# Kernel tuning notes

Measured on AMD Instinct MI355X. Metric: run time of the kernel, lower is better.

Reference implementation:

```python
import jax, jax.numpy as jnp
import numpy as np

N_HEAD = 16
NEG = 1e10


def setup_inputs() -> dict:
    key = jax.random.key(0)
    k1, k2, k3 = jax.random.split(key, 3)
    nx = 1024
    B, S = 2, 2048
    x = jax.random.normal(k1, (B, S, nx), dtype=jnp.float32)
    w_attn = jax.random.normal(k2, (nx, 3 * nx), dtype=jnp.float32) * (1.0 / np.sqrt(nx))
    b_attn = jnp.zeros((3 * nx,), dtype=jnp.float32)
    w_proj = jax.random.normal(k3, (nx, nx), dtype=jnp.float32) * (1.0 / np.sqrt(nx))
    b_proj = jnp.zeros((nx,), dtype=jnp.float32)
    return {"x": x, "w_attn": w_attn, "b_attn": b_attn, "w_proj": w_proj, "b_proj": b_proj}


def reference(x, w_attn, b_attn, w_proj, b_proj):
    B, S, nx = x.shape
    d = nx // N_HEAD
    qkv = x @ w_attn + b_attn                      # [B,S,3*nx]
    q, k, v = jnp.split(qkv, 3, axis=-1)
    # split heads: [B,S,nx] -> [B,H,S,d]
    q = q.reshape(B, S, N_HEAD, d).transpose(0, 2, 1, 3)
    k = k.reshape(B, S, N_HEAD, d).transpose(0, 2, 1, 3)
    v = v.reshape(B, S, N_HEAD, d).transpose(0, 2, 1, 3)
    # present: stack of (key stored as [B,H,S,d], value) like torch code
    present = jnp.stack((k, v))                    # [2,B,H,S,d]
    # scores with scale and additive causal mask (GPT-2 style: w*b - 1e10*(1-b))
    w = jnp.einsum('bhqd,bhkd->bhqk', q, k) / jnp.sqrt(jnp.float32(d))
    mask = jnp.tril(jnp.ones((S, S), dtype=w.dtype))[None, None]
    w = w * mask - NEG * (1.0 - mask)
    w = jax.nn.softmax(w, axis=-1)
    a = jnp.einsum('bhqk,bhkd->bhqd', w, v)        # [B,H,S,d]
    a = a.transpose(0, 2, 1, 3).reshape(B, S, nx)  # merge heads
    a = a @ w_proj + b_proj
    return (a, present)
```

## Files before the change

kernel.cpp:

```cpp
#include <hip/hip_runtime.h>
#include <stdint.h>
#include <stddef.h>

#define DEVI __device__ __forceinline__

typedef __bf16 bf16x8 __attribute__((ext_vector_type(8)));
typedef float  f32x4  __attribute__((ext_vector_type(4)));
typedef float  f32x16 __attribute__((ext_vector_type(16)));
typedef unsigned short u16;
typedef uint32_t u32;
typedef u16 u16x8 __attribute__((ext_vector_type(8)));
typedef u16 u16x4 __attribute__((ext_vector_type(4)));
typedef u32 u32x2 __attribute__((ext_vector_type(2)));
typedef u32 u32x4 __attribute__((ext_vector_type(4)));

typedef __attribute__((address_space(1))) void as1_void;
typedef __attribute__((address_space(3))) void as3_void;

static constexpr float SC = 0.18033688011112042f;

DEVI u16 f2bf(float f) {
  uint32_t u = __builtin_bit_cast(uint32_t, f);
  u += 0x7fffu + ((u >> 16) & 1u);
  return (u16)(u >> 16);
}

DEVI void gload_lds16(const void* g, void* l) {
  __builtin_amdgcn_global_load_lds((as1_void*)(void*)g, (as3_void*)l, 16, 0, 0);
}

#if __has_builtin(__builtin_amdgcn_exp2f)
DEVI float fast_exp2(float x) { return __builtin_amdgcn_exp2f(x); }
#else
DEVI float fast_exp2(float x) { return exp2f(x); }
#endif

DEVI u32 cvtpk(float lo, float hi) {
  u32 r;
  asm("v_cvt_pk_bf16_f32 %0, %1, %2" : "=v"(r) : "v"(lo), "v"(hi));
  return r;
}
DEVI void plswap(u32& a, u32& b) {
  asm("v_permlane32_swap_b32 %0, %1" : "+v"(a), "+v"(b));
}

__global__ __launch_bounds__(256) void k_cvt(const float* __restrict__ in,
                                             u16* __restrict__ out, int n) {
  int i = (blockIdx.x * 256 + threadIdx.x) * 4;
  if (i >= n) return;
  const float4 v = *(const float4*)(in + i);
  u16x4 o = { f2bf(v.x), f2bf(v.y), f2bf(v.z), f2bf(v.w) };
  *(u16x4*)(out + i) = o;
}

__global__ __launch_bounds__(256) void k_tcvt(const float* __restrict__ in,
                                              u16* __restrict__ out, int R, int C) {
  __shared__ float tile[32][33];
  const int c0 = blockIdx.x * 32, r0 = blockIdx.y * 32;
  const int tx = threadIdx.x, ty = threadIdx.y;
#pragma unroll
  for (int i = ty; i < 32; i += 8)
    tile[i][tx] = in[(size_t)(r0 + i) * C + (c0 + tx)];
  __syncthreads();
#pragma unroll
  for (int i = ty; i < 32; i += 8)
    out[(size_t)(c0 + i) * R + (r0 + tx)] = f2bf(tile[tx][i]);
}

__global__ __launch_bounds__(256) void k_vt(const u16* __restrict__ in,
                                            u16* __restrict__ out) {
  __shared__ u16 tile[64][72];
  const int tid = threadIdx.x;
  const int s0 = blockIdx.x * 64;
  const int bh = blockIdx.y;
  const size_t ib = (size_t)bh * 131072;
#pragma unroll
  for (int it = 0; it < 2; ++it) {
    const int r = (tid >> 3) + it * 32;
    const int c8 = (tid & 7) * 8;
    u16x8 v = *(const u16x8*)(in + ib + (size_t)(s0 + r) * 64 + c8);
    *(u16x8*)&tile[r][c8] = v;
  }
  __syncthreads();
#pragma unroll
  for (int it = 0; it < 2; ++it) {
    const int d = (tid >> 3) + it * 32;
    const int s8 = (tid & 7) * 8;
    u16x8 v;
#pragma unroll
    for (int jj = 0; jj < 8; ++jj) v[jj] = tile[s8 + jj][d];
    *(u16x8*)(out + ib + (size_t)d * 2048 + s0 + s8) = v;
  }
}

template <int EPI>
__global__ __launch_bounds__(256) void k_gemm(
    const u16* __restrict__ A, const u16* __restrict__ Bt,
    const float* __restrict__ bias,
    u16* __restrict__ wq, u16* __restrict__ wk, u16* __restrict__ wv,
    float* __restrict__ pk, float* __restrict__ pv, float* __restrict__ of) {
  constexpr int K = 1024;
  constexpr int NT = K / 32;
  __shared__ __align__(16) u16 Ash[3][128 * 32];
  __shared__ __align__(16) u16 Bsh[3][128 * 32];
  const int tid = threadIdx.x;
  const int lane = tid & 63, wid = tid >> 6;
  const int wm = wid >> 1, wn = wid & 1;
  const int lr = lane & 15, lg = lane >> 4;

  const int nwgx = gridDim.x;
  const int nwg = nwgx * gridDim.y;
  int lbid = blockIdx.y * nwgx + blockIdx.x;
  lbid = (lbid & 7) * (nwg >> 3) + (lbid >> 3);
  const int m0 = (lbid / nwgx) * 128, n0 = (lbid % nwgx) * 128;

  const int c = wid * 64 + lane;
  const u16* Ag1 = A + (size_t)(m0 + (c >> 2)) * K + (c & 3) * 8;
  const u16* Ag2 = A + (size_t)(m0 + 64 + (c >> 2)) * K + (c & 3) * 8;
  const u16* Bg1 = Bt + (size_t)(n0 + (c >> 2)) * K + (c & 3) * 8;
  const u16* Bg2 = Bt + (size_t)(n0 + 64 + (c >> 2)) * K + (c & 3) * 8;

  f32x4 acc[4][4];
#pragma unroll
  for (int i = 0; i < 4; ++i)
#pragma unroll
    for (int j = 0; j < 4; ++j) acc[i][j] = (f32x4)0.0f;

#define STAGE(sel, kk)                                        \
  {                                                           \
    gload_lds16(Ag1 + (kk), &Ash[sel][wid * 512]);            \
    gload_lds16(Ag2 + (kk), &Ash[sel][2048 + wid * 512]);     \
    gload_lds16(Bg1 + (kk), &Bsh[sel][wid * 512]);            \
    gload_lds16(Bg2 + (kk), &Bsh[sel][2048 + wid * 512]);     \
  }

  STAGE(0, 0)
  STAGE(1, 32)
  asm volatile("s_waitcnt vmcnt(4)" ::: "memory");
  __builtin_amdgcn_sched_barrier(0);
  __builtin_amdgcn_s_barrier();
  __builtin_amdgcn_sched_barrier(0);

  int cur = 0;
  for (int j = 0; j < NT; ++j) {
    const bool pf = (j + 2 < NT);
    int nb = cur + 2; if (nb >= 3) nb -= 3;
    if (pf) STAGE(nb, (j + 2) * 32)
    bf16x8 af[4], bfr[4];
#pragma unroll
    for (int f = 0; f < 4; ++f) {
      af[f]  = *(const bf16x8*)&Ash[cur][(wm * 64 + f * 16 + lr) * 32 + lg * 8];
      bfr[f] = *(const bf16x8*)&Bsh[cur][(wn * 64 + f * 16 + lr) * 32 + lg * 8];
    }
    __builtin_amdgcn_s_setprio(1);
#pragma unroll
    for (int i = 0; i < 4; ++i)
#pragma unroll
      for (int jj = 0; jj < 4; ++jj)
        acc[i][jj] = __builtin_amdgcn_mfma_f32_16x16x32_bf16(af[i], bfr[jj], acc[i][jj], 0, 0, 0);
    __builtin_amdgcn_s_setprio(0);
    if (pf) asm volatile("s_waitcnt vmcnt(4)" ::: "memory");
    else    asm volatile("s_waitcnt vmcnt(0)" ::: "memory");
    __builtin_amdgcn_sched_barrier(0);
    __builtin_amdgcn_s_barrier();
    __builtin_amdgcn_sched_barrier(0);
    cur = (cur + 1 == 3) ? 0 : cur + 1;
  }
#undef STAGE

  if constexpr (EPI == 0) {
#pragma unroll
    for (int j = 0; j < 4; ++j) {
      const int n = n0 + wn * 64 + j * 16 + lr;
      const float bv = bias[n];
      const int sec = n >> 10;
      const int nn = n & 1023;
      const int h = nn >> 6, dd = nn & 63;
#pragma unroll
      for (int i = 0; i < 4; ++i) {
        const int mb = m0 + wm * 64 + i * 16 + lg * 4;
        const int bb = mb >> 11, ss = mb & 2047;
        const size_t ib = (size_t)(bb * 16 + h) * 131072 + (size_t)ss * 64 + dd;
        if (sec == 0) {
#pragma unroll
          for (int r = 0; r < 4; ++r)
            wq[ib + (size_t)r * 64] = f2bf(acc[i][j][r] + bv);
        } else if (sec == 1) {
#pragma unroll
          for (int r = 0; r < 4; ++r) {
            const float v = acc[i][j][r] + bv;
            wk[ib + (size_t)r * 64] = f2bf(v);
            pk[ib + (size_t)r * 64] = v;
          }
        } else {
#pragma unroll
          for (int r = 0; r < 4; ++r) {
            const float v = acc[i][j][r] + bv;
            wv[ib + (size_t)r * 64] = f2bf(v);
            pv[ib + (size_t)r * 64] = v;
          }
        }
      }
    }
  } else {
#pragma unroll
    for (int j = 0; j < 4; ++j) {
      const int n = n0 + wn * 64 + j * 16 + lr;
      const float bv = bias[n];
#pragma unroll
      for (int i = 0; i < 4; ++i) {
        const int mb = m0 + wm * 64 + i * 16 + lg * 4;
#pragma unroll
        for (int r = 0; r < 4; ++r)
          of[(size_t)(mb + r) * 1024 + n] = acc[i][j][r] + bv;
      }
    }
  }
}

__global__ __launch_bounds__(128) void k_attn(const u16* __restrict__ Q,
                                              const u16* __restrict__ Kp,
                                              const u16* __restrict__ VT,
                                              u16* __restrict__ AO) {
  __shared__ __align__(16) u16 Ksh[2][4096];
  __shared__ __align__(16) u16 Vsh[2][4096];

  const int tid = threadIdx.x;
  const int lane = tid & 63, w = tid >> 6;
  const int l31 = lane & 31, hi = lane >> 5;
  const int bid = blockIdx.x;
  const int bh = bid & 31;
  const int j4 = bid >> 8;
  const int g  = (bid >> 5) & 7;
  const int qt = (j4 == 0) ? (31 - g) : (j4 == 1) ? g : (j4 == 2) ? (23 - g) : (8 + g);
  const int b = bh >> 4, h = bh & 15;
  const size_t hb = (size_t)bh * (2048 * 64);

  const int T = qt + 1;
  const int qb = qt * 64 + w * 32;

  const int srow = w * 32 + (lane >> 3);
  const int sslot = (lane & 7) ^ (lane >> 3);
  const u16* Kg = Kp + hb + (size_t)srow * 64 + sslot * 8;
  const u16* Vg = VT + hb + (size_t)srow * 2048 + sslot * 8;

#define STAGEA(sel, jt)                                                       \
  {                                                                           \
    gload_lds16(Kg + (size_t)(jt) * 4096,          &Ksh[sel][w * 2048]);      \
    gload_lds16(Kg + (size_t)(jt) * 4096 + 512,    &Ksh[sel][w * 2048 + 512]);\
    gload_lds16(Kg + (size_t)(jt) * 4096 + 1024,   &Ksh[sel][w * 2048 + 1024]);\
    gload_lds16(Kg + (size_t)(jt) * 4096 + 1536,   &Ksh[sel][w * 2048 + 1536]);\
    gload_lds16(Vg + (size_t)(jt) * 64,            &Vsh[sel][w * 2048]);      \
    gload_lds16(Vg + (size_t)(jt) * 64 + 16384,    &Vsh[sel][w * 2048 + 512]);\
    gload_lds16(Vg + (size_t)(jt) * 64 + 32768,    &Vsh[sel][w * 2048 + 1024]);\
    gload_lds16(Vg + (size_t)(jt) * 64 + 49152,    &Vsh[sel][w * 2048 + 1536]);\
  }

  const u16* Qp = Q + hb + (size_t)(qb + l31) * 64 + hi * 8;
  const bf16x8 qf0 = *(const bf16x8*)(Qp);
  const bf16x8 qf1 = *(const bf16x8*)(Qp + 16);
  const bf16x8 qf2 = *(const bf16x8*)(Qp + 32);
  const bf16x8 qf3 = *(const bf16x8*)(Qp + 48);

  f32x16 o0 = (f32x16)0.0f, o1 = (f32x16)0.0f;
  float mrun = -1e30f, lrun = 0.0f;

  const int xr = l31 & 7;

  STAGEA(0, 0)
  __syncthreads();

  int sel = 0;
  for (int jt = 0; jt < T; ++jt) {
    if (jt + 1 < T) STAGEA(sel ^ 1, jt + 1)
    const u16* Kb = Ksh[sel];
    const u16* Vb = Vsh[sel];
    bf16x8 kf[2][4];
#pragma unroll
    for (int s = 0; s < 2; ++s)
#pragma unroll
      for (int c = 0; c < 4; ++c)
        kf[s][c] = *(const bf16x8*)&Kb[(s * 32 + l31) * 64 + (((2 * c + hi) ^ xr) * 8)];

    f32x16 s0 = (f32x16)0.0f, s1 = (f32x16)0.0f;
    __builtin_amdgcn_s_setprio(1);
    s0 = __builtin_amdgcn_mfma_f32_32x32x16_bf16(kf[0][0], qf0, s0, 0, 0, 0);
    s1 = __builtin_amdgcn_mfma_f32_32x32x16_bf16(kf[1][0], qf0, s1, 0, 0, 0);
    s0 = __builtin_amdgcn_mfma_f32_32x32x16_bf16(kf[0][1], qf1, s0, 0, 0, 0);
    s1 = __builtin_amdgcn_mfma_f32_32x32x16_bf16(kf[1][1], qf1, s1, 0, 0, 0);
    s0 = __builtin_amdgcn_mfma_f32_32x32x16_bf16(kf[0][2], qf2, s0, 0, 0, 0);
    s1 = __builtin_amdgcn_mfma_f32_32x32x16_bf16(kf[1][2], qf2, s1, 0, 0, 0);
    s0 = __builtin_amdgcn_mfma_f32_32x32x16_bf16(kf[0][3], qf3, s0, 0, 0, 0);
    s1 = __builtin_amdgcn_mfma_f32_32x32x16_bf16(kf[1][3], qf3, s1, 0, 0, 0);
    __builtin_amdgcn_s_setprio(0);

    if (jt == T - 1) {
      const int qrel = w * 32 + l31;
      const int h4 = hi * 4;
#pragma unroll
      for (int r = 0; r < 16; ++r) {
        const int kp = (r & 3) + ((r >> 2) << 3) + h4;
        s0[r] = (kp <= qrel) ? s0[r] : -1e30f;
        s1[r] = (kp + 32 <= qrel) ? s1[r] : -1e30f;
      }
    }

    float t8[8];
#pragma unroll
    for (int r = 0; r < 8; ++r)
      t8[r] = fmaxf(fmaxf(s0[r], s0[r + 8]), fmaxf(s1[r], s1[r + 8]));
    float tm = fmaxf(fmaxf(fmaxf(t8[0], t8[1]), fmaxf(t8[2], t8[3])),
                     fmaxf(fmaxf(t8[4], t8[5]), fmaxf(t8[6], t8[7])));
    tm = fmaxf(tm, __shfl_xor(tm, 32));
    if (!__all(tm <= mrun)) {
      const float mnew = fmaxf(mrun, tm);
      const float al = fast_exp2((mrun - mnew) * SC);
      mrun = mnew;
      lrun *= al;
#pragma unroll
      for (int r = 0; r < 16; ++r) { o0[r] *= al; o1[r] *= al; }
    }
    const float nb2 = -mrun * SC;
#pragma unroll
    for (int r = 0; r < 16; ++r) {
      s0[r] = fast_exp2(fmaf(s0[r], SC, nb2));
      s1[r] = fast_exp2(fmaf(s1[r], SC, nb2));
    }
    float u8[8];
#pragma unroll
    for (int r = 0; r < 8; ++r)
      u8[r] = (s0[r] + s0[r + 8]) + (s1[r] + s1[r + 8]);
    lrun += ((u8[0] + u8[1]) + (u8[2] + u8[3])) + ((u8[4] + u8[5]) + (u8[6] + u8[7]));

    bf16x8 pb0, pb1, pb2, pb3;
#define PACK_CHUNK(sv, bb, dst)                                   \
    {                                                             \
      u32 a0 = cvtpk(sv[bb + 0], sv[bb + 1]);                     \
      u32 a1 = cvtpk(sv[bb + 2], sv[bb + 3]);                     \
      u32 a2 = cvtpk(sv[bb + 4], sv[bb + 5]);                     \
      u32 a3 = cvtpk(sv[bb + 6], sv[bb + 7]);                     \
      plswap(a0, a2);                                             \
      plswap(a1, a3);                                             \
      u32x4 fv = {a0, a1, a2, a3};                                \
      dst = __builtin_bit_cast(bf16x8, fv);                       \
    }
    PACK_CHUNK(s0, 0, pb0)
    PACK_CHUNK(s0, 8, pb1)
    PACK_CHUNK(s1, 0, pb2)
    PACK_CHUNK(s1, 8, pb3)
#undef PACK_CHUNK

    bf16x8 vf[2][4];
#pragma unroll
    for (int mt = 0; mt < 2; ++mt)
#pragma unroll
      for (int c = 0; c < 4; ++c)
        vf[mt][c] = *(const bf16x8*)&Vb[(mt * 32 + l31) * 64 + (((2 * c + hi) ^ xr) * 8)];

    __builtin_amdgcn_s_setprio(1);
    o0 = __builtin_amdgcn_mfma_f32_32x32x16_bf16(vf[0][0], pb0, o0, 0, 0, 0);
    o1 = __builtin_amdgcn_mfma_f32_32x32x16_bf16(vf[1][0], pb0, o1, 0, 0, 0);
    o0 = __builtin_amdgcn_mfma_f32_32x32x16_bf16(vf[0][1], pb1, o0, 0, 0, 0);
    o1 = __builtin_amdgcn_mfma_f32_32x32x16_bf16(vf[1][1], pb1, o1, 0, 0, 0);
    o0 = __builtin_amdgcn_mfma_f32_32x32x16_bf16(vf[0][2], pb2, o0, 0, 0, 0);
    o1 = __builtin_amdgcn_mfma_f32_32x32x16_bf16(vf[1][2], pb2, o1, 0, 0, 0);
    o0 = __builtin_amdgcn_mfma_f32_32x32x16_bf16(vf[0][3], pb3, o0, 0, 0, 0);
    o1 = __builtin_amdgcn_mfma_f32_32x32x16_bf16(vf[1][3], pb3, o1, 0, 0, 0);
    __builtin_amdgcn_s_setprio(0);

    __syncthreads();
    sel ^= 1;
  }
#undef STAGEA

  const float lt = lrun + __shfl_xor(lrun, 32);
  const float inv = 1.0f / lt;
  u16* aorow = AO + (size_t)(b * 2048 + qb + l31) * 1024 + h * 64 + hi * 4;
#pragma unroll
  for (int g2 = 0; g2 < 4; ++g2) {
    u32 w0 = cvtpk(o0[4 * g2 + 0] * inv, o0[4 * g2 + 1] * inv);
    u32 w1 = cvtpk(o0[4 * g2 + 2] * inv, o0[4 * g2 + 3] * inv);
    u32x2 ww = {w0, w1};
    *(u32x2*)(aorow + g2 * 8) = ww;
  }
#pragma unroll
  for (int g2 = 0; g2 < 4; ++g2) {
    u32 w0 = cvtpk(o1[4 * g2 + 0] * inv, o1[4 * g2 + 1] * inv);
    u32 w1 = cvtpk(o1[4 * g2 + 2] * inv, o1[4 * g2 + 3] * inv);
    u32x2 ww = {w0, w1};
    *(u32x2*)(aorow + 32 + g2 * 8) = ww;
  }
}

extern "C" void kernel_launch(void* const* d_in, const int* in_sizes, int n_in,
                              void* d_out, int out_size, void* d_ws, size_t ws_size,
                              hipStream_t stream) {
  const float* x      = (const float*)d_in[0];
  const float* w_attn = (const float*)d_in[1];
  const float* b_attn = (const float*)d_in[2];
  const float* w_proj = (const float*)d_in[3];
  const float* b_proj = (const float*)d_in[4];
  float* out = (float*)d_out;

  char* ws = (char*)d_ws;
  u16* x_bf  = (u16*)(ws);
  u16* wat_t = (u16*)(ws + 8388608);
  u16* wpj_t = (u16*)(ws + 14680064);
  u16* q_ws  = (u16*)(ws + 16777216);
  u16* k_ws  = (u16*)(ws + 25165824);
  u16* v_ws  = (u16*)(ws + 33554432);
  u16* a_ws  = (u16*)(ws + 41943040);
  u16* vT_ws = (u16*)(ws);

  k_cvt<<<4096, 256, 0, stream>>>(x, x_bf, 4194304);
  k_tcvt<<<dim3(96, 32), dim3(32, 8), 0, stream>>>(w_attn, wat_t, 1024, 3072);
  k_tcvt<<<dim3(32, 32), dim3(32, 8), 0, stream>>>(w_proj, wpj_t, 1024, 1024);

  k_gemm<0><<<dim3(24, 32), 256, 0, stream>>>(x_bf, wat_t, b_attn,
                                              q_ws, k_ws, v_ws,
                                              out + 4194304, out + 8388608, nullptr);

  k_vt<<<dim3(32, 32), 256, 0, stream>>>(v_ws, vT_ws);

  k_attn<<<dim3(1024), 128, 0, stream>>>(q_ws, k_ws, vT_ws, a_ws);

  k_gemm<1><<<dim3(8, 32), 256, 0, stream>>>(a_ws, wpj_t, b_proj,
                                             nullptr, nullptr, nullptr,
                                             nullptr, nullptr, out);
}
```

Baseline: 138.0 us.

## Split KV range across two waves per 32-row query tile with LDS merge

Restructures the attention kernel so each block handles two 32-row query tiles (paired for causal balance). The two waves split the key range of each tile and combine their partial softmax states through LDS. V is now loaded directly from global into registers with manual vmcnt waits instead of being staged through LDS. K staging becomes per-wave. The intent is better load balance, fewer block-wide barriers, and overlap of V loads with the QK/softmax work. The cost is an extra LDS merge and reliance on hand-tuned waitcnt counts. The launch grid in the unseen launcher must match the new block-to-tile mapping.

```diff
diff --git a/kernel.cpp b/kernel.cpp
--- a/kernel.cpp
+++ b/kernel.cpp
@@ -218,178 +218,237 @@
   }
 }
 
-__global__ __launch_bounds__(128) void k_attn(const u16* __restrict__ Q,
-                                              const u16* __restrict__ Kp,
-                                              const u16* __restrict__ VT,
-                                              u16* __restrict__ AO) {
-  __shared__ __align__(16) u16 Ksh[2][4096];
-  __shared__ __align__(16) u16 Vsh[2][4096];
+__global__ __launch_bounds__(128, 2) void k_attn(const u16* __restrict__ Q,
+                                                 const u16* __restrict__ Kp,
+                                                 const u16* __restrict__ VT,
+                                                 u16* __restrict__ AO) {
+  __shared__ __align__(16) u16 Ksh[2][2][4096];
 
   const int tid = threadIdx.x;
   const int lane = tid & 63, w = tid >> 6;
   const int l31 = lane & 31, hi = lane >> 5;
   const int bid = blockIdx.x;
   const int bh = bid & 31;
-  const int j4 = bid >> 8;
-  const int g  = (bid >> 5) & 7;
-  const int qt = (j4 == 0) ? (31 - g) : (j4 == 1) ? g : (j4 == 2) ? (23 - g) : (8 + g);
+  const int p = bid >> 5;
   const int b = bh >> 4, h = bh & 15;
   const size_t hb = (size_t)bh * (2048 * 64);
-
-  const int T = qt + 1;
-  const int qb = qt * 64 + w * 32;
-
-  const int srow = w * 32 + (lane >> 3);
-  const int sslot = (lane & 7) ^ (lane >> 3);
-  const u16* Kg = Kp + hb + (size_t)srow * 64 + sslot * 8;
-  const u16* Vg = VT + hb + (size_t)srow * 2048 + sslot * 8;
-
-#define STAGEA(sel, jt)                                                       \
-  {                                                                           \
-    gload_lds16(Kg + (size_t)(jt) * 4096,          &Ksh[sel][w * 2048]);      \
-    gload_lds16(Kg + (size_t)(jt) * 4096 + 512,    &Ksh[sel][w * 2048 + 512]);\
-    gload_lds16(Kg + (size_t)(jt) * 4096 + 1024,   &Ksh[sel][w * 2048 + 1024]);\
-    gload_lds16(Kg + (size_t)(jt) * 4096 + 1536,   &Ksh[sel][w * 2048 + 1536]);\
-    gload_lds16(Vg + (size_t)(jt) * 64,            &Vsh[sel][w * 2048]);      \
-    gload_lds16(Vg + (size_t)(jt) * 64 + 16384,    &Vsh[sel][w * 2048 + 512]);\
-    gload_lds16(Vg + (size_t)(jt) * 64 + 32768,    &Vsh[sel][w * 2048 + 1024]);\
-    gload_lds16(Vg + (size_t)(jt) * 64 + 49152,    &Vsh[sel][w * 2048 + 1536]);\
-  }
-
-  const u16* Qp = Q + hb + (size_t)(qb + l31) * 64 + hi * 8;
-  const bf16x8 qf0 = *(const bf16x8*)(Qp);
-  const bf16x8 qf1 = *(const bf16x8*)(Qp + 16);
-  const bf16x8 qf2 = *(const bf16x8*)(Qp + 32);
-  const bf16x8 qf3 = *(const bf16x8*)(Qp + 48);
-
-  f32x16 o0 = (f32x16)0.0f, o1 = (f32x16)0.0f;
-  float mrun = -1e30f, lrun = 0.0f;
-
   const int xr = l31 & 7;
 
-  STAGEA(0, 0)
-  __syncthreads();
-
-  int sel = 0;
-  for (int jt = 0; jt < T; ++jt) {
-    if (jt + 1 < T) STAGEA(sel ^ 1, jt + 1)
-    const u16* Kb = Ksh[sel];
-    const u16* Vb = Vsh[sel];
-    bf16x8 kf[2][4];
-#pragma unroll
-    for (int s = 0; s < 2; ++s)
-#pragma unroll
-      for (int c = 0; c < 4; ++c)
-        kf[s][c] = *(const bf16x8*)&Kb[(s * 32 + l31) * 64 + (((2 * c + hi) ^ xr) * 8)];
-
-    f32x16 s0 = (f32x16)0.0f, s1 = (f32x16)0.0f;
-    __builtin_amdgcn_s_setprio(1);
-    s0 = __builtin_amdgcn_mfma_f32_32x32x16_bf16(kf[0][0], qf0, s0, 0, 0, 0);
-    s1 = __builtin_amdgcn_mfma_f32_32x32x16_bf16(kf[1][0], qf0, s1, 0, 0, 0);
-    s0 = __builtin_amdgcn_mfma_f32_32x32x16_bf16(kf[0][1], qf1, s0, 0, 0, 0);
-    s1 = __builtin_amdgcn_mfma_f32_32x32x16_bf16(kf[1][1], qf1, s1, 0, 0, 0);
-    s0 = __builtin_amdgcn_mfma_f32_32x32x16_bf16(kf[0][2], qf2, s0, 0, 0, 0);
-    s1 = __builtin_amdgcn_mfma_f32_32x32x16_bf16(kf[1][2], qf2, s1, 0, 0, 0);
-    s0 = __builtin_amdgcn_mfma_f32_32x32x16_bf16(kf[0][3], qf3, s0, 0, 0, 0);
-    s1 = __builtin_amdgcn_mfma_f32_32x32x16_bf16(kf[1][3], qf3, s1, 0, 0, 0);
-    __builtin_amdgcn_s_setprio(0);
-
-    if (jt == T - 1) {
-      const int qrel = w * 32 + l31;
-      const int h4 = hi * 4;
+  const u16* Kg = Kp + hb + (size_t)(lane >> 3) * 64 + (size_t)(((lane & 7) ^ (lane >> 3)) * 8);
+  const u16* Vg = VT + hb + (size_t)l31 * 2048 + hi * 8;
+
+  float* OslB = (float*)&Ksh[0][0][0];
+  float* ML   = (float*)&Ksh[0][1][0];
+
+#define STAGEK(sel, jt)                                       \
+  {                                                           \
+    u16* kd = &Ksh[w][sel][0];                                \
+    const u16* ks = Kg + (size_t)(jt) * 4096;                 \
+    gload_lds16(ks,        kd);                               \
+    gload_lds16(ks +  512, kd +  512);                        \
+    gload_lds16(ks + 1024, kd + 1024);                        \
+    gload_lds16(ks + 1536, kd + 1536);                        \
+    gload_lds16(ks + 2048, kd + 2048);                        \
+    gload_lds16(ks + 2560, kd + 2560);                        \
+    gload_lds16(ks + 3072, kd + 3072);                        \
+    gload_lds16(ks + 3584, kd + 3584);                        \
+  }
+
+#define GL16(dst, ptr, IMM)                                           \
+  asm volatile("global_load_dwordx4 %0, %1, off offset:" #IMM         \
+               : "=v"(dst) : "v"(ptr));
+
+#define LOADV(jt)                                             \
+  {                                                           \
+    const u16* vp0 = Vg + (size_t)(jt) * 64;                  \
+    const u16* vp1 = vp0 + 65536;                             \
+    GL16(vv[0][0], vp0, 0)  GL16(vv[0][1], vp0, 32)           \
+    GL16(vv[0][2], vp0, 64) GL16(vv[0][3], vp0, 96)           \
+    GL16(vv[1][0], vp1, 0)  GL16(vv[1][1], vp1, 32)           \
+    GL16(vv[1][2], vp1, 64) GL16(vv[1][3], vp1, 96)           \
+  }
+
+  for (int t = 0; t < 2; ++t) {
+    const int qtl = t ? (63 - p) : p;
+    const int T = (qtl >> 1) + 1;
+    const int mid = (T + 1) >> 1;
+    const int lo  = w ? mid : 0;
+    const int hiE = w ? T : mid;
+    const int qb = qtl * 32;
+
+    const u16* Qp2 = Q + hb + (size_t)(qb + l31) * 64 + hi * 8;
+    const bf16x8 qf0 = *(const bf16x8*)(Qp2);
+    const bf16x8 qf1 = *(const bf16x8*)(Qp2 + 16);
+    const bf16x8 qf2 = *(const bf16x8*)(Qp2 + 32);
+    const bf16x8 qf3 = *(const bf16x8*)(Qp2 + 48);
+
+    f32x16 o0 = (f32x16)0.0f, o1 = (f32x16)0.0f;
+    float mrun = -1e30f, lrun = 0.0f;
+
+    if (lo < hiE) {
+      STAGEK(0, lo)
+      int cur = 0;
+      for (int jt = lo; jt < hiE; ++jt) {
+        const bool hn = (jt + 1 < hiE);
+        u32x4 vv[2][4];
+        LOADV(jt)
+        if (hn) STAGEK(cur ^ 1, jt + 1)
+        if (hn) asm volatile("s_waitcnt vmcnt(16)" ::: "memory");
+        else    asm volatile("s_waitcnt vmcnt(8)"  ::: "memory");
+        __builtin_amdgcn_sched_barrier(0);
+
+        const u16* Kb = &Ksh[w][cur][0];
+        bf16x8 kf[2][4];
+#pragma unroll
+        for (int s = 0; s < 2; ++s)
+#pragma unroll
+          for (int c = 0; c < 4; ++c)
+            kf[s][c] = *(const bf16x8*)&Kb[(s * 32 + l31) * 64 + (((2 * c + hi) ^ xr) * 8)];
+
+        f32x16 s0 = (f32x16)0.0f, s1 = (f32x16)0.0f;
+        __builtin_amdgcn_s_setprio(1);
+        s0 = __builtin_amdgcn_mfma_f32_32x32x16_bf16(kf[0][0], qf0, s0, 0, 0, 0);
+        s1 = __builtin_amdgcn_mfma_f32_32x32x16_bf16(kf[1][0], qf0, s1, 0, 0, 0);
+        s0 = __builtin_amdgcn_mfma_f32_32x32x16_bf16(kf[0][1], qf1, s0, 0, 0, 0);
+        s1 = __builtin_amdgcn_mfma_f32_32x32x16_bf16(kf[1][1], qf1, s1, 0, 0, 0);
+        s0 = __builtin_amdgcn_mfma_f32_32x32x16_bf16(kf[0][2], qf2, s0, 0, 0, 0);
+        s1 = __builtin_amdgcn_mfma_f32_32x32x16_bf16(kf[1][2], qf2, s1, 0, 0, 0);
+        s0 = __builtin_amdgcn_mfma_f32_32x32x16_bf16(kf[0][3], qf3, s0, 0, 0, 0);
+        s1 = __builtin_amdgcn_mfma_f32_32x32x16_bf16(kf[1][3], qf3, s1, 0, 0, 0);
+        __builtin_amdgcn_s_setprio(0);
+
+        if (jt == T - 1) {
+          const int qrel = (qtl & 1) * 32 + l31;
+          const int h4 = hi * 4;
+#pragma unroll
+          for (int r = 0; r < 16; ++r) {
+            const int kp = (r & 3) + ((r >> 2) << 3) + h4;
+            s0[r] = (kp <= qrel) ? s0[r] : -1e30f;
+            s1[r] = (kp + 32 <= qrel) ? s1[r] : -1e30f;
+          }
+        }
+
+        float t8[8];
+#pragma unroll
+        for (int r = 0; r < 8; ++r)
+          t8[r] = fmaxf(fmaxf(s0[r], s0[r + 8]), fmaxf(s1[r], s1[r + 8]));
+        float tm = fmaxf(fmaxf(fmaxf(t8[0], t8[1]), fmaxf(t8[2], t8[3])),
+                         fmaxf(fmaxf(t8[4], t8[5]), fmaxf(t8[6], t8[7])));
+        tm = fmaxf(tm, __shfl_xor(tm, 32));
+        if (!__all(tm <= mrun)) {
+          const float mnew = fmaxf(mrun, tm);
+          const float al = fast_exp2((mrun - mnew) * SC);
+          mrun = mnew;
+          lrun *= al;
+#pragma unroll
+          for (int r = 0; r < 16; ++r) { o0[r] *= al; o1[r] *= al; }
+        }
+        const float nb2 = -mrun * SC;
+#pragma unroll
+        for (int r = 0; r < 16; ++r) {
+          s0[r] = fast_exp2(fmaf(s0[r], SC, nb2));
+          s1[r] = fast_exp2(fmaf(s1[r], SC, nb2));
+        }
+        float u8[8];
+#pragma unroll
+        for (int r = 0; r < 8; ++r)
+          u8[r] = (s0[r] + s0[r + 8]) + (s1[r] + s1[r + 8]);
+        lrun += ((u8[0] + u8[1]) + (u8[2] + u8[3])) + ((u8[4] + u8[5]) + (u8[6] + u8[7]));
+
+        bf16x8 pb0, pb1, pb2, pb3;
+#define PACK_CHUNK(sv, bb, dst)                                   \
+        {                                                         \
+          u32 a0 = cvtpk(sv[bb + 0], sv[bb + 1]);                 \
+          u32 a1 = cvtpk(sv[bb + 2], sv[bb + 3]);                 \
+          u32 a2 = cvtpk(sv[bb + 4], sv[bb + 5]);                 \
+          u32 a3 = cvtpk(sv[bb + 6], sv[bb + 7]);                 \
+          plswap(a0, a2);                                         \
+          plswap(a1, a3);                                         \
+          u32x4 fv = {a0, a1, a2, a3};                            \
+          dst = __builtin_bit_cast(bf16x8, fv);                   \
+        }
+        PACK_CHUNK(s0, 0, pb0)
+        PACK_CHUNK(s0, 8, pb1)
+        PACK_CHUNK(s1, 0, pb2)
+        PACK_CHUNK(s1, 8, pb3)
+#undef PACK_CHUNK
+
+        if (hn) asm volatile("s_waitcnt vmcnt(8)" ::: "memory");
+        else    asm volatile("s_waitcnt vmcnt(0)" ::: "memory");
+        __builtin_amdgcn_sched_barrier(0);
+
+        const bf16x8 vf00 = __builtin_bit_cast(bf16x8, vv[0][0]);
+        const bf16x8 vf01 = __builtin_bit_cast(bf16x8, vv[0][1]);
+        const bf16x8 vf02 = __builtin_bit_cast(bf16x8, vv[0][2]);
+        const bf16x8 vf03 = __builtin_bit_cast(bf16x8, vv[0][3]);
+        const bf16x8 vf10 = __builtin_bit_cast(bf16x8, vv[1][0]);
+        const bf16x8 vf11 = __builtin_bit_cast(bf16x8, vv[1][1]);
+        const bf16x8 vf12 = __builtin_bit_cast(bf16x8, vv[1][2]);
+        const bf16x8 vf13 = __builtin_bit_cast(bf16x8, vv[1][3]);
+
+        __builtin_amdgcn_s_setprio(1);
+        o0 = __builtin_amdgcn_mfma_f32_32x32x16_bf16(vf00, pb0, o0, 0, 0, 0);
+        o1 = __builtin_amdgcn_mfma_f32_32x32x16_bf16(vf10, pb0, o1, 0, 0, 0);
+        o0 = __builtin_amdgcn_mfma_f32_32x32x16_bf16(vf01, pb1, o0, 0, 0, 0);
+        o1 = __builtin_amdgcn_mfma_f32_32x32x16_bf16(vf11, pb1, o1, 0, 0, 0);
+        o0 = __builtin_amdgcn_mfma_f32_32x32x16_bf16(vf02, pb2, o0, 0, 0, 0);
+        o1 = __builtin_amdgcn_mfma_f32_32x32x16_bf16(vf12, pb2, o1, 0, 0, 0);
+        o0 = __builtin_amdgcn_mfma_f32_32x32x16_bf16(vf03, pb3, o0, 0, 0, 0);
+        o1 = __builtin_amdgcn_mfma_f32_32x32x16_bf16(vf13, pb3, o1, 0, 0, 0);
+        __builtin_amdgcn_s_setprio(0);
+
+        cur ^= 1;
+      }
+    }
+
+    __syncthreads();
+    if (w == 1) {
 #pragma unroll
       for (int r = 0; r < 16; ++r) {
-        const int kp = (r & 3) + ((r >> 2) << 3) + h4;
-        s0[r] = (kp <= qrel) ? s0[r] : -1e30f;
-        s1[r] = (kp + 32 <= qrel) ? s1[r] : -1e30f;
-      }
-    }
-
-    float t8[8];
-#pragma unroll
-    for (int r = 0; r < 8; ++r)
-      t8[r] = fmaxf(fmaxf(s0[r], s0[r + 8]), fmaxf(s1[r], s1[r + 8]));
-    float tm = fmaxf(fmaxf(fmaxf(t8[0], t8[1]), fmaxf(t8[2], t8[3])),
-                     fmaxf(fmaxf(t8[4], t8[5]), fmaxf(t8[6], t8[7])));
-    tm = fmaxf(tm, __shfl_xor(tm, 32));
-    if (!__all(tm <= mrun)) {
-      const float mnew = fmaxf(mrun, tm);
-      const float al = fast_exp2((mrun - mnew) * SC);
-      mrun = mnew;
-      lrun *= al;
-#pragma unroll
-      for (int r = 0; r < 16; ++r) { o0[r] *= al; o1[r] *= al; }
-    }
-    const float nb2 = -mrun * SC;
-#pragma unroll
-    for (int r = 0; r < 16; ++r) {
-      s0[r] = fast_exp2(fmaf(s0[r], SC, nb2));
-      s1[r] = fast_exp2(fmaf(s1[r], SC, nb2));
-    }
-    float u8[8];
-#pragma unroll
-    for (int r = 0; r < 8; ++r)
-      u8[r] = (s0[r] + s0[r + 8]) + (s1[r] + s1[r + 8]);
-    lrun += ((u8[0] + u8[1]) + (u8[2] + u8[3])) + ((u8[4] + u8[5]) + (u8[6] + u8[7]));
-
-    bf16x8 pb0, pb1, pb2, pb3;
-#define PACK_CHUNK(sv, bb, dst)                                   \
-    {                                                             \
-      u32 a0 = cvtpk(sv[bb + 0], sv[bb + 1]);                     \
-      u32 a1 = cvtpk(sv[bb + 2], sv[bb + 3]);                     \
-      u32 a2 = cvtpk(sv[bb + 4], sv[bb + 5]);                     \
-      u32 a3 = cvtpk(sv[bb + 6], sv[bb + 7]);                     \
-      plswap(a0, a2);                                             \
-      plswap(a1, a3);                                             \
-      u32x4 fv = {a0, a1, a2, a3};                                \
-      dst = __builtin_bit_cast(bf16x8, fv);                       \
-    }
-    PACK_CHUNK(s0, 0, pb0)
-    PACK_CHUNK(s0, 8, pb1)
-    PACK_CHUNK(s1, 0, pb2)
-    PACK_CHUNK(s1, 8, pb3)
-#undef PACK_CHUNK
-
-    bf16x8 vf[2][4];
-#pragma unroll
-    for (int mt = 0; mt < 2; ++mt)
-#pragma unroll
-      for (int c = 0; c < 4; ++c)
-        vf[mt][c] = *(const bf16x8*)&Vb[(mt * 32 + l31) * 64 + (((2 * c + hi) ^ xr) * 8)];
-
-    __builtin_amdgcn_s_setprio(1);
-    o0 = __builtin_amdgcn_mfma_f32_32x32x16_bf16(vf[0][0], pb0, o0, 0, 0, 0);
-    o1 = __builtin_amdgcn_mfma_f32_32x32x16_bf16(vf[1][0], pb0, o1, 0, 0, 0);
-    o0 = __builtin_amdgcn_mfma_f32_32x32x16_bf16(vf[0][1], pb1, o0, 0, 0, 0);
-    o1 = __builtin_amdgcn_mfma_f32_32x32x16_bf16(vf[1][1], pb1, o1, 0, 0, 0);
-    o0 = __builtin_amdgcn_mfma_f32_32x32x16_bf16(vf[0][2], pb2, o0, 0, 0, 0);
-    o1 = __builtin_amdgcn_mfma_f32_32x32x16_bf16(vf[1][2], pb2, o1, 0, 0, 0);
-    o0 = __builtin_amdgcn_mfma_f32_32x32x16_bf16(vf[0][3], pb3, o0, 0, 0, 0);
-    o1 = __builtin_amdgcn_mfma_f32_32x32x16_bf16(vf[1][3], pb3, o1, 0, 0, 0);
-    __builtin_amdgcn_s_setprio(0);
-
+        OslB[r * 64 + lane]        = o0[r];
+        OslB[(16 + r) * 64 + lane] = o1[r];
+      }
+      ML[lane]      = mrun;
+      ML[64 + lane] = lrun;
+    }
     __syncthreads();
-    sel ^= 1;
-  }
-#undef STAGEA
-
-  const float lt = lrun + __shfl_xor(lrun, 32);
-  const float inv = 1.0f / lt;
-  u16* aorow = AO + (size_t)(b * 2048 + qb + l31) * 1024 + h * 64 + hi * 4;
-#pragma unroll
-  for (int g2 = 0; g2 < 4; ++g2) {
-    u32 w0 = cvtpk(o0[4 * g2 + 0] * inv, o0[4 * g2 + 1] * inv);
-    u32 w1 = cvtpk(o0[4 * g2 + 2] * inv, o0[4 * g2 + 3] * inv);
-    u32x2 ww = {w0, w1};
-    *(u32x2*)(aorow + g2 * 8) = ww;
-  }
-#pragma unroll
-  for (int g2 = 0; g2 < 4; ++g2) {
-    u32 w0 = cvtpk(o1[4 * g2 + 0] * inv, o1[4 * g2 + 1] * inv);
-    u32 w1 = cvtpk(o1[4 * g2 + 2] * inv, o1[4 * g2 + 3] * inv);
-    u32x2 ww = {w0, w1};
-    *(u32x2*)(aorow + 32 + g2 * 8) = ww;
-  }
+    if (w == 0) {
+      const float mB = ML[lane];
+      const float lB = ML[64 + lane];
+      const float m  = fmaxf(mrun, mB);
+      const float al = fast_exp2((mrun - m) * SC);
+      const float bt = fast_exp2((mB - m) * SC);
+      lrun = lrun * al + lB * bt;
+#pragma unroll
+      for (int r = 0; r < 16; ++r) {
+        o0[r] = o0[r] * al + OslB[r * 64 + lane] * bt;
+        o1[r] = o1[r] * al + OslB[(16 + r) * 64 + lane] * bt;
+      }
+
+      const float lt = lrun + __shfl_xor(lrun, 32);
+      const float inv = 1.0f / lt;
+      u16* aorow = AO + (size_t)(b * 2048 + qb + l31) * 1024 + h * 64 + hi * 4;
+#pragma unroll
+      for (int g2 = 0; g2 < 4; ++g2) {
+        u32 w0s = cvtpk(o0[4 * g2 + 0] * inv, o0[4 * g2 + 1] * inv);
+        u32 w1s = cvtpk(o0[4 * g2 + 2] * inv, o0[4 * g2 + 3] * inv);
+        u32x2 ww = {w0s, w1s};
+        *(u32x2*)(aorow + g2 * 8) = ww;
+      }
+#pragma unroll
+      for (int g2 = 0; g2 < 4; ++g2) {
+        u32 w0s = cvtpk(o1[4 * g2 + 0] * inv, o1[4 * g2 + 1] * inv);
+        u32 w1s = cvtpk(o1[4 * g2 + 2] * inv, o1[4 * g2 + 3] * inv);
+        u32x2 ww = {w0s, w1s};
+        *(u32x2*)(aorow + 32 + g2 * 8) = ww;
+      }
+      asm volatile("s_waitcnt lgkmcnt(0)" ::: "memory");
+      __builtin_amdgcn_sched_barrier(0);
+    }
+  }
+#undef STAGEK
+#undef LOADV
+#undef GL16
 }
 
 extern "C" void kernel_launch(void* const* d_in, const int* in_sizes, int n_in,
```

After: 135.5 us. Within noise of the previous version (-1.7%).
